# Performance work log

Measured on AMD Instinct MI355X. Metric: run time of the kernel, lower is better.

## Reference

```python
import jax, jax.numpy as jnp
import numpy as np

N_NODES = 50000


def _gcn_layer(x, edge_index, W, b, relu):
    """tf_geometric-style GCN: h = D^-1/2 (A+I) D^-1/2 (x @ W) + b, opt relu."""
    n = x.shape[0]
    h = x @ W  # [N, D_out] transform first (standard GCN)
    src, dst = edge_index[0], edge_index[1]
    sl = jnp.arange(n, dtype=src.dtype)
    src = jnp.concatenate([src, sl])  # add self-loops (renorm trick)
    dst = jnp.concatenate([dst, sl])
    deg = jax.ops.segment_sum(jnp.ones_like(dst, dtype=h.dtype), dst, num_segments=n)
    dinv = jax.lax.rsqrt(jnp.maximum(deg, 1e-12))
    norm = dinv[src] * dinv[dst]  # symmetric normalization per edge
    msg = h[src] * norm[:, None]  # [E+N, D_out] gather + scale
    out = jax.ops.segment_sum(msg, dst, num_segments=n) + b
    return jax.nn.relu(out) if relu else out


def setup_inputs() -> dict:
    key = jax.random.key(0)
    ks = jax.random.split(key, 12)
    F, E = 512, 800000
    d = {}
    d["x"] = jax.random.normal(ks[0], (N_NODES, F), dtype=jnp.float32)
    d["edge_index1"] = jax.random.randint(ks[1], (2, E), 0, N_NODES, dtype=jnp.int32)
    d["edge_index2"] = jax.random.randint(ks[2], (2, E), 0, N_NODES, dtype=jnp.int32)
    def glorot(k, shape):
        lim = np.sqrt(6.0 / (shape[0] + shape[1])).astype(np.float32)
        return jax.random.uniform(k, shape, jnp.float32, -lim, lim)
    d["W10"] = glorot(ks[3], (F, 256)); d["b10"] = jnp.zeros((256,), jnp.float32)
    d["W20"] = glorot(ks[4], (F, 64));  d["b20"] = jnp.zeros((64,), jnp.float32)
    d["W21"] = glorot(ks[5], (64, 256)); d["b21"] = jnp.zeros((256,), jnp.float32)
    d["Wfc"] = glorot(ks[6], (256, 16)); d["bfc"] = jnp.zeros((16,), jnp.float32)
    return d


def reference(x, edge_index1, edge_index2, W10, b10, W20, b20, W21, b21, Wfc, bfc):
    h1 = _gcn_layer(x, edge_index1, W10, b10, relu=True)   # GCN(256, relu)
    h2 = _gcn_layer(x, edge_index2, W20, b20, relu=False)  # GCN(64)
    h2 = _gcn_layer(h2, edge_index2, W21, b21, relu=True)  # GCN(256, relu)
    h = h1 + h2
    return h @ Wfc + bfc  # Dense(class_num)
```

## Files before the change

kernel.cpp:

```cpp
#include <hip/hip_runtime.h>
#include <hip/hip_bf16.h>
#include <cstdint>
#include <cstddef>

#define N_NODES 50000
#define FDIM 512
#define NBKT 391
#define CHUNK 8192
#define BCAP 4096

typedef __bf16 bf16_t;
typedef bf16_t bf16x8 __attribute__((ext_vector_type(8)));
typedef float f32x4 __attribute__((ext_vector_type(4)));

__device__ __forceinline__ unsigned short f2bf(float f) {
  union { float f; uint32_t u; } c; c.f = f;
  uint32_t u = c.u;
  uint32_t r = (u + 0x7fffu + ((u >> 16) & 1u)) >> 16;
  return (unsigned short)r;
}
__device__ __forceinline__ float bf2f(unsigned short u) {
  union { uint32_t i; float f; } c; c.i = (uint32_t)u << 16; return c.f;
}
__device__ __forceinline__ float4 ld_bf4(const unsigned short* p) {
  ushort4 u = *(const ushort4*)p;
  float4 r; r.x = bf2f(u.x); r.y = bf2f(u.y); r.z = bf2f(u.z); r.w = bf2f(u.w);
  return r;
}
__device__ __forceinline__ void async16(const void* g, void* l) {
  __builtin_amdgcn_global_load_lds((const __attribute__((address_space(1))) void*)g,
                                   (__attribute__((address_space(3))) void*)l, 16, 0, 0);
}

__global__ __launch_bounds__(256) void binA(const int* __restrict__ d1, const int* __restrict__ d2,
                                            int* __restrict__ M1, int* __restrict__ M2,
                                            int E1, int E2, int nch1, int nch2) {
  const int g = blockIdx.y;
  const int* dst = g ? d2 : d1;
  int* M = g ? M2 : M1;
  const int E = g ? E2 : E1;
  const int nch = g ? nch2 : nch1;
  const int chunk = blockIdx.x;
  if (chunk >= nch) return;
  __shared__ int cnt[NBKT];
  for (int j = threadIdx.x; j < NBKT; j += 256) cnt[j] = 0;
  __syncthreads();
  const int base = chunk * CHUNK;
#pragma unroll 4
  for (int i = 0; i < CHUNK / 256; i++) {
    int e = base + i * 256 + threadIdx.x;
    if (e < E) atomicAdd(&cnt[dst[e] >> 7], 1);
  }
  __syncthreads();
  for (int j = threadIdx.x; j < NBKT; j += 256) M[chunk * NBKT + j] = cnt[j];
}

__global__ __launch_bounds__(512) void bin_offsets(int* __restrict__ M1, int* __restrict__ M2,
                                                   int* __restrict__ bases,
                                                   int nch1, int nch2, int E1, int E2) {
  const int g = blockIdx.x;
  int* M = g ? M2 : M1;
  const int nch = g ? nch2 : nch1;
  int* base = bases + g * (NBKT + 1);
  const int E = g ? E2 : E1;
  const int t = threadIdx.x;
  __shared__ int tot[512];
  int running = 0;
  if (t < NBKT) {
    for (int b = 0; b < nch; b++) {
      int v = M[b * NBKT + t];
      M[b * NBKT + t] = running;
      running += v;
    }
  }
  tot[t] = (t < NBKT) ? running : 0;
  __syncthreads();
  for (int off = 1; off < 512; off <<= 1) {
    int u = (t >= off) ? tot[t - off] : 0;
    __syncthreads();
    tot[t] += u;
    __syncthreads();
  }
  int ex = (t == 0) ? 0 : tot[t - 1];
  if (t < NBKT) {
    base[t] = ex;
    for (int b = 0; b < nch; b++) M[b * NBKT + t] += ex;
  }
  if (t == NBKT) base[NBKT] = E;
}

__global__ __launch_bounds__(256) void binB(const int* __restrict__ s1, const int* __restrict__ d1,
                                            const int* __restrict__ M1, unsigned* __restrict__ eb1,
                                            int E1, int nch1,
                                            const int* __restrict__ s2, const int* __restrict__ d2,
                                            const int* __restrict__ M2, unsigned* __restrict__ eb2,
                                            int E2, int nch2) {
  const int g = blockIdx.y;
  const int* src = g ? s2 : s1;
  const int* dst = g ? d2 : d1;
  const int* M = g ? M2 : M1;
  unsigned* eb = g ? eb2 : eb1;
  const int E = g ? E2 : E1;
  const int nch = g ? nch2 : nch1;
  const int chunk = blockIdx.x;
  if (chunk >= nch) return;
  __shared__ int gbase[NBKT];
  __shared__ int cur[NBKT];
  for (int j = threadIdx.x; j < NBKT; j += 256) {
    gbase[j] = M[chunk * NBKT + j];
    cur[j] = 0;
  }
  __syncthreads();
  const int base = chunk * CHUNK;
#pragma unroll 4
  for (int i = 0; i < CHUNK / 256; i++) {
    int e = base + i * 256 + threadIdx.x;
    if (e < E) {
      int d = dst[e];
      int b = d >> 7;
      int pos = gbase[b] + atomicAdd(&cur[b], 1);
      eb[pos] = ((unsigned)d << 16) | (unsigned)src[e];
    }
  }
}

__global__ __launch_bounds__(256) void binC(const unsigned* __restrict__ eb1,
                                            const unsigned* __restrict__ eb2,
                                            const int* __restrict__ bases,
                                            int* __restrict__ rp1, float* __restrict__ dv1,
                                            int* __restrict__ cs1,
                                            int* __restrict__ rp2, float* __restrict__ dv2,
                                            int* __restrict__ cs2, int n) {
  const int g = blockIdx.y;
  const unsigned* eb = g ? eb2 : eb1;
  const int* base = bases + g * (NBKT + 1);
  int* rp = g ? rp2 : rp1;
  float* dv = g ? dv2 : dv1;
  int* cs = g ? cs2 : cs1;
  const int bkt = blockIdx.x;
  const int e0 = base[bkt], e1 = base[bkt + 1];
  const int cnt = e1 - e0;
  const int node0 = bkt << 7;
  const int t = threadIdx.x;
  __shared__ unsigned stage[BCAP];
  __shared__ int sorted[BCAP];
  __shared__ int dcnt[128], dcur[128], dscan[128];
  if (t < 128) dcnt[t] = 0;
  __syncthreads();
  for (int i = t; i < cnt; i += 256) {
    unsigned pe = eb[e0 + i];
    stage[i] = pe;
    atomicAdd(&dcnt[(pe >> 16) & 127], 1);
  }
  __syncthreads();
  if (t < 128) dscan[t] = dcnt[t];
  __syncthreads();
  for (int off = 1; off < 128; off <<= 1) {
    int u = (t < 128 && t >= off) ? dscan[t - off] : 0;
    __syncthreads();
    if (t < 128) dscan[t] += u;
    __syncthreads();
  }
  if (t < 128) {
    int ex = dscan[t] - dcnt[t];
    dcur[t] = ex;
    int node = node0 + t;
    if (node < n) {
      rp[node] = e0 + ex;
      dv[node] = rsqrtf((float)dcnt[t] + 1.0f);
    }
  }
  __syncthreads();
  for (int i = t; i < cnt; i += 256) {
    unsigned pe = stage[i];
    int d = (pe >> 16) & 127;
    int pos = atomicAdd(&dcur[d], 1);
    sorted[pos] = (int)(pe & 0xFFFFu);
  }
  __syncthreads();
  for (int i = t; i < cnt; i += 256) cs[e0 + i] = sorted[i];
  if (bkt == NBKT - 1 && t == 0) rp[n] = base[NBKT];
}

__global__ void cvt_x(const float4* __restrict__ X, ushort4* __restrict__ out, int n4) {
  int stride = gridDim.x * 256;
  for (int i = blockIdx.x * 256 + threadIdx.x; i < n4; i += stride) {
    float4 v = X[i];
    ushort4 o;
    o.x = f2bf(v.x); o.y = f2bf(v.y); o.z = f2bf(v.z); o.w = f2bf(v.w);
    out[i] = o;
  }
}

__global__ void cvt_w(const float* __restrict__ W10, const float* __restrict__ W20,
                      const float* __restrict__ W21, unsigned short* __restrict__ WcatT,
                      unsigned short* __restrict__ W21T) {
  int j = blockIdx.x * 256 + threadIdx.x;
  const int T1 = 384 * 512;
  if (j < T1) {
    int n = j >> 9, k = j & 511;
    float v = (n < 256) ? W10[k * 256 + n] : ((n < 320) ? W20[k * 64 + (n - 256)] : 0.f);
    WcatT[j] = f2bf(v);
  } else {
    int j2 = j - T1;
    if (j2 < 256 * 64) {
      int n = j2 >> 6, k = j2 & 63;
      W21T[j2] = f2bf(W21[k * 256 + n]);
    }
  }
}

template <int KTOT, int SPLIT>
__global__ __launch_bounds__(256) void gemm_bt(const unsigned short* __restrict__ A,
                                               const unsigned short* __restrict__ B,
                                               void* __restrict__ o1, void* __restrict__ o2,
                                               int M, int NLIM) {
  __shared__ unsigned short As[128 * 64];
  __shared__ unsigned short Bs[128 * 64];
  const int tid = threadIdx.x;
  const int w = tid >> 6, lane = tid & 63;
  const int row0 = blockIdx.x * 128;
  const int n0 = blockIdx.y * 128;
  const int wm = w >> 1, wn = w & 1;
  const int lr = lane >> 3, lc8 = (lane & 7) * 8;
  const int mlane = lane & 15, q = lane >> 4;

  f32x4 acc[4][4];
#pragma unroll
  for (int mi = 0; mi < 4; mi++)
#pragma unroll
    for (int ni = 0; ni < 4; ni++) {
      f32x4 z = {0.f, 0.f, 0.f, 0.f};
      acc[mi][ni] = z;
    }

  for (int k0 = 0; k0 < KTOT; k0 += 64) {
    __syncthreads();
#pragma unroll
    for (int i = 0; i < 4; i++) {
      int gr = row0 + i * 32 + w * 8 + lr;
      if (gr > M - 1) gr = M - 1;
      async16(A + (size_t)gr * KTOT + k0 + lc8, &As[(i * 32 + w * 8) * 64]);
    }
#pragma unroll
    for (int i = 0; i < 4; i++) {
      int n = i * 32 + w * 8 + lr;
      async16(B + (size_t)(n0 + n) * KTOT + k0 + lc8, &Bs[(i * 32 + w * 8) * 64]);
    }
    __syncthreads();
#pragma unroll
    for (int kk = 0; kk < 2; kk++) {
      bf16x8 af[4], bfr[4];
#pragma unroll
      for (int mi = 0; mi < 4; mi++)
        af[mi] = *(const bf16x8*)&As[(wm * 64 + mi * 16 + mlane) * 64 + kk * 32 + q * 8];
#pragma unroll
      for (int ni = 0; ni < 4; ni++)
        bfr[ni] = *(const bf16x8*)&Bs[(wn * 64 + ni * 16 + mlane) * 64 + kk * 32 + q * 8];
#pragma unroll
      for (int mi = 0; mi < 4; mi++)
#pragma unroll
        for (int ni = 0; ni < 4; ni++)
          acc[mi][ni] = __builtin_amdgcn_mfma_f32_16x16x32_bf16(af[mi], bfr[ni], acc[mi][ni], 0, 0, 0);
    }
  }

#pragma unroll
  for (int mi = 0; mi < 4; mi++)
#pragma unroll
    for (int ni = 0; ni < 4; ni++) {
      int c = n0 + wn * 64 + ni * 16 + mlane;
#pragma unroll
      for (int rg = 0; rg < 4; rg++) {
        int r = row0 + wm * 64 + mi * 16 + q * 4 + rg;
        if (r < M) {
          float v = acc[mi][ni][rg];
          if (SPLIT) {
            if (c < 256) ((unsigned short*)o1)[(size_t)r * 256 + c] = f2bf(v);
            else if (c < NLIM) ((unsigned short*)o2)[(size_t)r * 64 + (c - 256)] = f2bf(v);
          } else {
            ((float*)o1)[(size_t)r * 256 + c] = v;
          }
        }
      }
    }
}

__global__ __launch_bounds__(256) void prop256(const unsigned short* __restrict__ H,
                                               const int* __restrict__ rp,
                                               const int* __restrict__ cs,
                                               const float* __restrict__ dinv,
                                               const float* __restrict__ bias,
                                               float* __restrict__ out, int n) {
  const int i = blockIdx.x * 4 + (threadIdx.x >> 6);
  const int l = threadIdx.x & 63;
  if (i >= n) return;
  const float di = dinv[i];
  float4 self = ld_bf4(H + (size_t)i * 256 + l * 4);
  float4 acc;
  acc.x = di * self.x; acc.y = di * self.y; acc.z = di * self.z; acc.w = di * self.w;
  const int e1 = rp[i + 1];
#pragma unroll 4
  for (int e = rp[i]; e < e1; e++) {
    int s = cs[e];
    float wgt = dinv[s];
    float4 rrow = ld_bf4(H + (size_t)s * 256 + l * 4);
    acc.x += wgt * rrow.x; acc.y += wgt * rrow.y; acc.z += wgt * rrow.z; acc.w += wgt * rrow.w;
  }
  float4 b = *(const float4*)(bias + l * 4);
  float4 o;
  o.x = fmaxf(di * acc.x + b.x, 0.f);
  o.y = fmaxf(di * acc.y + b.y, 0.f);
  o.z = fmaxf(di * acc.z + b.z, 0.f);
  o.w = fmaxf(di * acc.w + b.w, 0.f);
  *(float4*)(out + (size_t)i * 256 + l * 4) = o;
}

template <int BIAS>
__global__ __launch_bounds__(256) void prop64(const unsigned short* __restrict__ H,
                                              const int* __restrict__ rp,
                                              const int* __restrict__ cs,
                                              const float* __restrict__ dinv,
                                              const float* __restrict__ bias,
                                              unsigned short* __restrict__ out, int n) {
  const int i = blockIdx.x * 16 + (threadIdx.x >> 4);
  const int l = threadIdx.x & 15;
  if (i >= n) return;
  const float di = dinv[i];
  float4 self = ld_bf4(H + (size_t)i * 64 + l * 4);
  float4 acc;
  acc.x = di * self.x; acc.y = di * self.y; acc.z = di * self.z; acc.w = di * self.w;
  const int e1 = rp[i + 1];
#pragma unroll 4
  for (int e = rp[i]; e < e1; e++) {
    int s = cs[e];
    float wgt = dinv[s];
    float4 rrow = ld_bf4(H + (size_t)s * 64 + l * 4);
    acc.x += wgt * rrow.x; acc.y += wgt * rrow.y; acc.z += wgt * rrow.z; acc.w += wgt * rrow.w;
  }
  float4 o;
  o.x = di * acc.x; o.y = di * acc.y; o.z = di * acc.z; o.w = di * acc.w;
  if (BIAS) {
    float4 b = *(const float4*)(bias + l * 4);
    o.x += b.x; o.y += b.y; o.z += b.z; o.w += b.w;
  }
  ushort4 ob;
  ob.x = f2bf(o.x); ob.y = f2bf(o.y); ob.z = f2bf(o.z); ob.w = f2bf(o.w);
  *(ushort4*)(out + (size_t)i * 64 + l * 4) = ob;
}

__global__ __launch_bounds__(256) void final_k(const float* __restrict__ h1,
                                               const float* __restrict__ h3,
                                               const float* __restrict__ b21,
                                               const float* __restrict__ Wfc,
                                               const float* __restrict__ bfc,
                                               float* __restrict__ out, int M) {
  __shared__ float hs[16][260];
  __shared__ float wt[16][260];
  __shared__ float bs[16];
  const int t = threadIdx.x;
  for (int j = t; j < 4096; j += 256) { int k = j >> 4, c = j & 15; wt[c][k] = Wfc[j]; }
  if (t < 16) bs[t] = bfc[t];
  const float bb = b21[t];
  const int node0 = blockIdx.x * 16;
#pragma unroll
  for (int nl = 0; nl < 16; nl++) {
    int i = node0 + nl;
    float v = 0.f;
    if (i < M) {
      size_t o = (size_t)i * 256 + t;
      v = fmaxf(h3[o] + bb, 0.f) + h1[o];
    }
    hs[nl][t] = v;
  }
  __syncthreads();
  const int nl = t >> 4, c = t & 15;
  const int i = node0 + nl;
  if (i >= M) return;
  const float4* hp = (const float4*)&hs[nl][0];
  const float4* wp = (const float4*)&wt[c][0];
  float s = bs[c];
#pragma unroll 8
  for (int k4 = 0; k4 < 64; k4++) {
    float4 a = hp[k4], b = wp[k4];
    s += a.x * b.x + a.y * b.y + a.z * b.z + a.w * b.w;
  }
  out[(size_t)i * 16 + c] = s;
}

extern "C" void kernel_launch(void* const* d_in, const int* in_sizes, int n_in,
                              void* d_out, int out_size, void* d_ws, size_t ws_size,
                              hipStream_t stream) {
  const float* X   = (const float*)d_in[0];
  const int*   ei1 = (const int*)d_in[1];
  const int*   ei2 = (const int*)d_in[2];
  const float* W10 = (const float*)d_in[3];
  const float* b10 = (const float*)d_in[4];
  const float* W20 = (const float*)d_in[5];
  const float* b20 = (const float*)d_in[6];
  const float* W21 = (const float*)d_in[7];
  const float* b21 = (const float*)d_in[8];
  const float* Wfc = (const float*)d_in[9];
  const float* bfc = (const float*)d_in[10];
  float* out = (float*)d_out;

  const int N = N_NODES;
  const int E1 = in_sizes[1] / 2, E2 = in_sizes[2] / 2;
  const int* src1 = ei1; const int* dst1 = ei1 + E1;
  const int* src2 = ei2; const int* dst2 = ei2 + E2;
  const int nch1 = (E1 + CHUNK - 1) / CHUNK, nch2 = (E2 + CHUNK - 1) / CHUNK;
  const int nchmax = (nch1 > nch2) ? nch1 : nch2;

  char* p = (char*)d_ws;
  auto alloc = [&](size_t b) { char* r = p; p += (b + 255) & ~(size_t)255; return (void*)r; };
  int* M1 = (int*)alloc((size_t)nch1 * NBKT * 4);
  int* M2 = (int*)alloc((size_t)nch2 * NBKT * 4);
  int* bases = (int*)alloc((size_t)2 * (NBKT + 1) * 4);
  unsigned* eb1 = (unsigned*)alloc((size_t)E1 * 4);
  unsigned* eb2 = (unsigned*)alloc((size_t)E2 * 4);
  int* rp1 = (int*)alloc((size_t)(N + 1) * 4);
  int* rp2 = (int*)alloc((size_t)(N + 1) * 4);
  float* dinv1 = (float*)alloc((size_t)N * 4);
  float* dinv2 = (float*)alloc((size_t)N * 4);
  int* csr1s = (int*)alloc((size_t)E1 * 4);
  int* csr2s = (int*)alloc((size_t)E2 * 4);
  unsigned short* WcatT = (unsigned short*)alloc(384 * 512 * 2);
  unsigned short* W21T  = (unsigned short*)alloc(256 * 64 * 2);
  unsigned short* Xb = (unsigned short*)alloc((size_t)N * 512 * 2);
  float* h1 = (float*)Xb;
  unsigned short* Xh1b = (unsigned short*)alloc((size_t)N * 256 * 2);
  unsigned short* Xh2b = (unsigned short*)alloc((size_t)N * 64 * 2);
  unsigned short* h2b  = (unsigned short*)alloc((size_t)N * 64 * 2);
  unsigned short* q2b  = (unsigned short*)alloc((size_t)N * 64 * 2);
  float* h3 = (float*)alloc((size_t)N * 256 * 4);

  binA<<<dim3(nchmax, 2), 256, 0, stream>>>(dst1, dst2, M1, M2, E1, E2, nch1, nch2);
  bin_offsets<<<dim3(2), 512, 0, stream>>>(M1, M2, bases, nch1, nch2, E1, E2);
  binB<<<dim3(nchmax, 2), 256, 0, stream>>>(src1, dst1, M1, eb1, E1, nch1,
                                            src2, dst2, M2, eb2, E2, nch2);
  binC<<<dim3(NBKT, 2), 256, 0, stream>>>(eb1, eb2, bases, rp1, dinv1, csr1s,
                                          rp2, dinv2, csr2s, N);
  cvt_x<<<dim3(4096), 256, 0, stream>>>((const float4*)X, (ushort4*)Xb, N * FDIM / 4);
  cvt_w<<<dim3((384 * 512 + 256 * 64 + 255) / 256), 256, 0, stream>>>(W10, W20, W21, WcatT, W21T);
  gemm_bt<512, 1><<<dim3((N + 127) / 128, 3), 256, 0, stream>>>(Xb, WcatT, Xh1b, Xh2b, N, 320);
  prop256<<<dim3((N + 3) / 4), 256, 0, stream>>>(Xh1b, rp1, csr1s, dinv1, b10, h1, N);
  prop64<1><<<dim3((N + 15) / 16), 256, 0, stream>>>(Xh2b, rp2, csr2s, dinv2, b20, h2b, N);
  prop64<0><<<dim3((N + 15) / 16), 256, 0, stream>>>(h2b, rp2, csr2s, dinv2, nullptr, q2b, N);
  gemm_bt<64, 0><<<dim3((N + 127) / 128, 2), 256, 0, stream>>>(q2b, W21T, h3, nullptr, N, 256);
  final_k<<<dim3((N + 15) / 16), 256, 0, stream>>>(h1, h3, b21, Wfc, bfc, out, N);
}
```

Before: 469.4 us.

## Fuse X conversion into first GEMM and fuse second GEMM with final dense

Removes the separate fp32-to-bf16 conversion of X by having the first GEMM load fp32 rows directly, convert them into a 64x512 shared tile, and loop over all three output column blocks. The second small GEMM (q2 @ W21) is fused with bias, relu, the h1 add and the final 256x16 dense layer, so the fp32 h3 intermediate is never written or reread. The cost is larger shared-memory use, which lowers occupancy. Staging B is also serialized over three column passes per block.

```diff
diff --git a/kernel.cpp b/kernel.cpp
--- a/kernel.cpp
+++ b/kernel.cpp
@@ -182,16 +182,6 @@
   if (bkt == NBKT - 1 && t == 0) rp[n] = base[NBKT];
 }
 
-__global__ void cvt_x(const float4* __restrict__ X, ushort4* __restrict__ out, int n4) {
-  int stride = gridDim.x * 256;
-  for (int i = blockIdx.x * 256 + threadIdx.x; i < n4; i += stride) {
-    float4 v = X[i];
-    ushort4 o;
-    o.x = f2bf(v.x); o.y = f2bf(v.y); o.z = f2bf(v.z); o.w = f2bf(v.w);
-    out[i] = o;
-  }
-}
-
 __global__ void cvt_w(const float* __restrict__ W10, const float* __restrict__ W20,
                       const float* __restrict__ W21, unsigned short* __restrict__ WcatT,
                       unsigned short* __restrict__ W21T) {
@@ -210,80 +200,78 @@
   }
 }
 
-template <int KTOT, int SPLIT>
-__global__ __launch_bounds__(256) void gemm_bt(const unsigned short* __restrict__ A,
-                                               const unsigned short* __restrict__ B,
-                                               void* __restrict__ o1, void* __restrict__ o2,
-                                               int M, int NLIM) {
-  __shared__ unsigned short As[128 * 64];
-  __shared__ unsigned short Bs[128 * 64];
+__global__ __launch_bounds__(256) void xw512(const float* __restrict__ X,
+                                             const unsigned short* __restrict__ B,
+                                             unsigned short* __restrict__ o1,
+                                             unsigned short* __restrict__ o2, int M) {
+  __shared__ __attribute__((aligned(16))) unsigned short As[64 * 512];
+  __shared__ __attribute__((aligned(16))) unsigned short Bs[128 * 64];
   const int tid = threadIdx.x;
   const int w = tid >> 6, lane = tid & 63;
-  const int row0 = blockIdx.x * 128;
-  const int n0 = blockIdx.y * 128;
+  const int row0 = blockIdx.x * 64;
   const int wm = w >> 1, wn = w & 1;
-  const int lr = lane >> 3, lc8 = (lane & 7) * 8;
   const int mlane = lane & 15, q = lane >> 4;
 
-  f32x4 acc[4][4];
-#pragma unroll
-  for (int mi = 0; mi < 4; mi++)
-#pragma unroll
-    for (int ni = 0; ni < 4; ni++) {
-      f32x4 z = {0.f, 0.f, 0.f, 0.f};
-      acc[mi][ni] = z;
-    }
-
-  for (int k0 = 0; k0 < KTOT; k0 += 64) {
-    __syncthreads();
-#pragma unroll
-    for (int i = 0; i < 4; i++) {
-      int gr = row0 + i * 32 + w * 8 + lr;
-      if (gr > M - 1) gr = M - 1;
-      async16(A + (size_t)gr * KTOT + k0 + lc8, &As[(i * 32 + w * 8) * 64]);
-    }
-#pragma unroll
-    for (int i = 0; i < 4; i++) {
-      int n = i * 32 + w * 8 + lr;
-      async16(B + (size_t)(n0 + n) * KTOT + k0 + lc8, &Bs[(i * 32 + w * 8) * 64]);
-    }
-    __syncthreads();
-#pragma unroll
-    for (int kk = 0; kk < 2; kk++) {
-      bf16x8 af[4], bfr[4];
-#pragma unroll
-      for (int mi = 0; mi < 4; mi++)
-        af[mi] = *(const bf16x8*)&As[(wm * 64 + mi * 16 + mlane) * 64 + kk * 32 + q * 8];
-#pragma unroll
-      for (int ni = 0; ni < 4; ni++)
-        bfr[ni] = *(const bf16x8*)&Bs[(wn * 64 + ni * 16 + mlane) * 64 + kk * 32 + q * 8];
-#pragma unroll
-      for (int mi = 0; mi < 4; mi++)
+#pragma unroll 4
+  for (int i = 0; i < 32; i++) {
+    int j = i * 256 + tid;
+    int row = j >> 7, col4 = j & 127;
+    int gr = row0 + row; if (gr > M - 1) gr = M - 1;
+    float4 v = *(const float4*)(X + (size_t)gr * 512 + col4 * 4);
+    ushort4 o; o.x = f2bf(v.x); o.y = f2bf(v.y); o.z = f2bf(v.z); o.w = f2bf(v.w);
+    *(ushort4*)&As[row * 512 + col4 * 4] = o;
+  }
+
+  for (int y = 0; y < 3; y++) {
+    f32x4 acc[2][4];
+#pragma unroll
+    for (int mi = 0; mi < 2; mi++)
+#pragma unroll
+      for (int ni = 0; ni < 4; ni++) {
+        f32x4 z = {0.f, 0.f, 0.f, 0.f};
+        acc[mi][ni] = z;
+      }
+    for (int k = 0; k < 8; k++) {
+      __syncthreads();
+#pragma unroll
+      for (int i = 0; i < 4; i++) {
+        int n = i * 32 + w * 8 + (lane >> 3);
+        async16(B + (size_t)(y * 128 + n) * 512 + k * 64 + (lane & 7) * 8,
+                &Bs[(i * 32 + w * 8) * 64]);
+      }
+      __syncthreads();
+#pragma unroll
+      for (int kk = 0; kk < 2; kk++) {
+        bf16x8 af[2], bfr[4];
+#pragma unroll
+        for (int mi = 0; mi < 2; mi++)
+          af[mi] = *(const bf16x8*)&As[(wm * 32 + mi * 16 + mlane) * 512 + k * 64 + kk * 32 + q * 8];
 #pragma unroll
         for (int ni = 0; ni < 4; ni++)
-          acc[mi][ni] = __builtin_amdgcn_mfma_f32_16x16x32_bf16(af[mi], bfr[ni], acc[mi][ni], 0, 0, 0);
-    }
-  }
-
-#pragma unroll
-  for (int mi = 0; mi < 4; mi++)
-#pragma unroll
-    for (int ni = 0; ni < 4; ni++) {
-      int c = n0 + wn * 64 + ni * 16 + mlane;
-#pragma unroll
-      for (int rg = 0; rg < 4; rg++) {
-        int r = row0 + wm * 64 + mi * 16 + q * 4 + rg;
-        if (r < M) {
-          float v = acc[mi][ni][rg];
-          if (SPLIT) {
-            if (c < 256) ((unsigned short*)o1)[(size_t)r * 256 + c] = f2bf(v);
-            else if (c < NLIM) ((unsigned short*)o2)[(size_t)r * 64 + (c - 256)] = f2bf(v);
-          } else {
-            ((float*)o1)[(size_t)r * 256 + c] = v;
+          bfr[ni] = *(const bf16x8*)&Bs[(wn * 64 + ni * 16 + mlane) * 64 + kk * 32 + q * 8];
+#pragma unroll
+        for (int mi = 0; mi < 2; mi++)
+#pragma unroll
+          for (int ni = 0; ni < 4; ni++)
+            acc[mi][ni] = __builtin_amdgcn_mfma_f32_16x16x32_bf16(af[mi], bfr[ni], acc[mi][ni], 0, 0, 0);
+      }
+    }
+#pragma unroll
+    for (int mi = 0; mi < 2; mi++)
+#pragma unroll
+      for (int ni = 0; ni < 4; ni++) {
+        int c = y * 128 + wn * 64 + ni * 16 + mlane;
+#pragma unroll
+        for (int rg = 0; rg < 4; rg++) {
+          int r = row0 + wm * 32 + mi * 16 + q * 4 + rg;
+          if (r < M) {
+            float v = acc[mi][ni][rg];
+            if (c < 256) o1[(size_t)r * 256 + c] = f2bf(v);
+            else if (c < 320) o2[(size_t)r * 64 + (c - 256)] = f2bf(v);
           }
         }
       }
-    }
+  }
 }
 
 __global__ __launch_bounds__(256) void prop256(const unsigned short* __restrict__ H,
@@ -349,43 +337,99 @@
   *(ushort4*)(out + (size_t)i * 64 + l * 4) = ob;
 }
 
-__global__ __launch_bounds__(256) void final_k(const float* __restrict__ h1,
-                                               const float* __restrict__ h3,
-                                               const float* __restrict__ b21,
-                                               const float* __restrict__ Wfc,
-                                               const float* __restrict__ bfc,
-                                               float* __restrict__ out, int M) {
-  __shared__ float hs[16][260];
-  __shared__ float wt[16][260];
-  __shared__ float bs[16];
-  const int t = threadIdx.x;
-  for (int j = t; j < 4096; j += 256) { int k = j >> 4, c = j & 15; wt[c][k] = Wfc[j]; }
-  if (t < 16) bs[t] = bfc[t];
-  const float bb = b21[t];
-  const int node0 = blockIdx.x * 16;
-#pragma unroll
-  for (int nl = 0; nl < 16; nl++) {
-    int i = node0 + nl;
-    float v = 0.f;
-    if (i < M) {
-      size_t o = (size_t)i * 256 + t;
-      v = fmaxf(h3[o] + bb, 0.f) + h1[o];
-    }
-    hs[nl][t] = v;
-  }
-  __syncthreads();
-  const int nl = t >> 4, c = t & 15;
-  const int i = node0 + nl;
-  if (i >= M) return;
-  const float4* hp = (const float4*)&hs[nl][0];
-  const float4* wp = (const float4*)&wt[c][0];
-  float s = bs[c];
+__global__ __launch_bounds__(512) void gf(const unsigned short* __restrict__ A,
+                                          const unsigned short* __restrict__ Bb,
+                                          const float* __restrict__ h1,
+                                          const float* __restrict__ b21,
+                                          const float* __restrict__ Wfc,
+                                          const float* __restrict__ bfc,
+                                          float* __restrict__ out, int M) {
+  __shared__ __attribute__((aligned(16))) float hsm[128 * 260];
+  __shared__ __attribute__((aligned(16))) float wt[256 * 16];
+  unsigned short* As = (unsigned short*)hsm;
+  unsigned short* Bs = As + 128 * 64;
+  const int tid = threadIdx.x;
+  const int w = tid >> 6, lane = tid & 63;
+  const int row0 = blockIdx.x * 128;
+  const int wm = w >> 2, wn = w & 3;
+  const int mlane = lane & 15, q = lane >> 4;
+
+  for (int j = tid; j < 4096; j += 512) wt[j] = Wfc[j];
+#pragma unroll
+  for (int i = 0; i < 2; i++) {
+    int gr = row0 + i * 64 + w * 8 + (lane >> 3);
+    if (gr > M - 1) gr = M - 1;
+    async16(A + (size_t)gr * 64 + (lane & 7) * 8, &As[(i * 64 + w * 8) * 64]);
+  }
+#pragma unroll
+  for (int i = 0; i < 4; i++) {
+    int n = i * 64 + w * 8 + (lane >> 3);
+    async16(Bb + (size_t)n * 64 + (lane & 7) * 8, &Bs[(i * 64 + w * 8) * 64]);
+  }
+  __syncthreads();
+
+  f32x4 acc[4][4];
+#pragma unroll
+  for (int mi = 0; mi < 4; mi++)
+#pragma unroll
+    for (int ni = 0; ni < 4; ni++) {
+      f32x4 z = {0.f, 0.f, 0.f, 0.f};
+      acc[mi][ni] = z;
+    }
+#pragma unroll
+  for (int kk = 0; kk < 2; kk++) {
+    bf16x8 af[4], bfr[4];
+#pragma unroll
+    for (int mi = 0; mi < 4; mi++)
+      af[mi] = *(const bf16x8*)&As[(wm * 64 + mi * 16 + mlane) * 64 + kk * 32 + q * 8];
+#pragma unroll
+    for (int ni = 0; ni < 4; ni++)
+      bfr[ni] = *(const bf16x8*)&Bs[(wn * 64 + ni * 16 + mlane) * 64 + kk * 32 + q * 8];
+#pragma unroll
+    for (int mi = 0; mi < 4; mi++)
+#pragma unroll
+      for (int ni = 0; ni < 4; ni++)
+        acc[mi][ni] = __builtin_amdgcn_mfma_f32_16x16x32_bf16(af[mi], bfr[ni], acc[mi][ni], 0, 0, 0);
+  }
+  __syncthreads();
+
+#pragma unroll
+  for (int ni = 0; ni < 4; ni++) {
+    int c = wn * 64 + ni * 16 + mlane;
+    float bb = b21[c];
+#pragma unroll
+    for (int mi = 0; mi < 4; mi++)
+#pragma unroll
+      for (int rg = 0; rg < 4; rg++) {
+        int rl = wm * 64 + mi * 16 + q * 4 + rg;
+        int gr = row0 + rl;
+        int grc = (gr < M) ? gr : (M - 1);
+        float v = fmaxf(acc[mi][ni][rg] + bb, 0.f) + h1[(size_t)grc * 256 + c];
+        hsm[rl * 260 + c] = v;
+      }
+  }
+  __syncthreads();
+
+  const int r = tid >> 2, j0 = (tid & 3) * 4;
+  const int gr = row0 + r;
+  if (gr < M) {
+    float4 s = *(const float4*)(bfc + j0);
+    const float* hrow = &hsm[r * 260];
 #pragma unroll 8
-  for (int k4 = 0; k4 < 64; k4++) {
-    float4 a = hp[k4], b = wp[k4];
-    s += a.x * b.x + a.y * b.y + a.z * b.z + a.w * b.w;
-  }
-  out[(size_t)i * 16 + c] = s;
+    for (int c4 = 0; c4 < 64; c4++) {
+      float4 h4 = *(const float4*)(hrow + c4 * 4);
+      const float* wp = &wt[(c4 * 4) * 16 + j0];
+      float4 a0 = *(const float4*)(wp);
+      float4 a1 = *(const float4*)(wp + 16);
+      float4 a2 = *(const float4*)(wp + 32);
+      float4 a3 = *(const float4*)(wp + 48);
+      s.x += h4.x * a0.x + h4.y * a1.x + h4.z * a2.x + h4.w * a3.x;
+      s.y += h4.x * a0.y + h4.y * a1.y + h4.z * a2.y + h4.w * a3.y;
+      s.z += h4.x * a0.z + h4.y * a1.z + h4.z * a2.z + h4.w * a3.z;
+      s.w += h4.x * a0.w + h4.y * a1.w + h4.z * a2.w + h4.w * a3.w;
+    }
+    *(float4*)(out + (size_t)gr * 16 + j0) = s;
+  }
 }
 
 extern "C" void kernel_launch(void* const* d_in, const int* in_sizes, int n_in,
@@ -426,13 +470,11 @@
   int* csr2s = (int*)alloc((size_t)E2 * 4);
   unsigned short* WcatT = (unsigned short*)alloc(384 * 512 * 2);
   unsigned short* W21T  = (unsigned short*)alloc(256 * 64 * 2);
-  unsigned short* Xb = (unsigned short*)alloc((size_t)N * 512 * 2);
-  float* h1 = (float*)Xb;
   unsigned short* Xh1b = (unsigned short*)alloc((size_t)N * 256 * 2);
   unsigned short* Xh2b = (unsigned short*)alloc((size_t)N * 64 * 2);
   unsigned short* h2b  = (unsigned short*)alloc((size_t)N * 64 * 2);
   unsigned short* q2b  = (unsigned short*)alloc((size_t)N * 64 * 2);
-  float* h3 = (float*)alloc((size_t)N * 256 * 4);
+  float* h1 = (float*)alloc((size_t)N * 256 * 4);
 
   binA<<<dim3(nchmax, 2), 256, 0, stream>>>(dst1, dst2, M1, M2, E1, E2, nch1, nch2);
   bin_offsets<<<dim3(2), 512, 0, stream>>>(M1, M2, bases, nch1, nch2, E1, E2);
@@ -440,12 +482,10 @@
                                             src2, dst2, M2, eb2, E2, nch2);
   binC<<<dim3(NBKT, 2), 256, 0, stream>>>(eb1, eb2, bases, rp1, dinv1, csr1s,
                                           rp2, dinv2, csr2s, N);
-  cvt_x<<<dim3(4096), 256, 0, stream>>>((const float4*)X, (ushort4*)Xb, N * FDIM / 4);
   cvt_w<<<dim3((384 * 512 + 256 * 64 + 255) / 256), 256, 0, stream>>>(W10, W20, W21, WcatT, W21T);
-  gemm_bt<512, 1><<<dim3((N + 127) / 128, 3), 256, 0, stream>>>(Xb, WcatT, Xh1b, Xh2b, N, 320);
+  xw512<<<dim3((N + 63) / 64), 256, 0, stream>>>(X, WcatT, Xh1b, Xh2b, N);
   prop256<<<dim3((N + 3) / 4), 256, 0, stream>>>(Xh1b, rp1, csr1s, dinv1, b10, h1, N);
   prop64<1><<<dim3((N + 15) / 16), 256, 0, stream>>>(Xh2b, rp2, csr2s, dinv2, b20, h2b, N);
   prop64<0><<<dim3((N + 15) / 16), 256, 0, stream>>>(h2b, rp2, csr2s, dinv2, nullptr, q2b, N);
-  gemm_bt<64, 0><<<dim3((N + 127) / 128, 2), 256, 0, stream>>>(q2b, W21T, h3, nullptr, N, 256);
-  final_k<<<dim3((N + 15) / 16), 256, 0, stream>>>(h1, h3, b21, Wfc, bfc, out, N);
-}
+  gf<<<dim3((N + 127) / 128), 512, 0, stream>>>(q2b, W21T, h1, b21, Wfc, bfc, out, N);
+}
```

Result: faster. 446.2 us (-4.9%).
